# Kernel optimization log

Measured on AMD Instinct MI355X. Metric: run time of the kernel, lower is better.

The kernel has to match this reference:

```python
import jax, jax.numpy as jnp
import numpy as np

SR = 48000.0
HARMONIC_NUM = 8
DIM = HARMONIC_NUM + 1
SINE_AMP = 0.1
NOISE_STD = 0.003
VOICED_THRESHOLD = 0.0


def setup_inputs() -> dict:
    key = jax.random.key(0)
    k1, k2, k3, k4 = jax.random.split(key, 4)
    B, L, upp = 4, 1000, 512
    Lo = L * upp
    f0 = jax.random.uniform(k1, (B, L), dtype=jnp.float32, minval=80.0, maxval=400.0)
    voiced = jax.random.uniform(k2, (B, L)) > 0.2
    f0 = f0 * voiced.astype(jnp.float32)
    rand_ini = jax.random.uniform(k3, (B, DIM), dtype=jnp.float32)
    noise_randn = jax.random.normal(k4, (B, Lo, DIM), dtype=jnp.float32)
    return {"f0": f0, "rand_ini": rand_ini, "noise_randn": noise_randn, "upp": upp}


def _linear_upsample_align_corners(x, upp):
    # x: (B, L, D) -> (B, L*upp, D), matches F.interpolate(mode='linear', align_corners=True)
    B, L, D = x.shape
    Lo = L * upp
    pos = jnp.arange(Lo, dtype=jnp.float32) * (jnp.float32(L - 1) / jnp.float32(Lo - 1))
    i0 = jnp.clip(jnp.floor(pos).astype(jnp.int32), 0, L - 2)
    frac = (pos - i0.astype(jnp.float32))[None, :, None]
    return x[:, i0, :] * (1.0 - frac) + x[:, i0 + 1, :] * frac


def reference(f0, rand_ini, noise_randn, upp):
    B, L = f0.shape
    Lo = L * upp
    # harmonics: f0, 2*f0, ..., DIM*f0  -> (B, L, DIM)
    f0_buf = f0[:, :, None] * jnp.arange(1, DIM + 1, dtype=f0.dtype)
    rad_values = (f0_buf / SR) % 1.0
    # random initial phase, first harmonic fixed at 0
    ri = rand_ini.at[:, 0].set(0.0)
    rad_values = rad_values.at[:, 0, :].add(ri)
    # cumulative phase at frame rate, scaled and upsampled
    tmp_over_one = jnp.cumsum(rad_values, axis=1) * upp
    tmp_over_one = _linear_upsample_align_corners(tmp_over_one, upp)  # (B, Lo, DIM)
    rad_up = jnp.repeat(rad_values, upp, axis=1)  # nearest upsample (B, Lo, DIM)
    tmp_over_one = tmp_over_one % 1.0
    # detect wrap-around and inject -1 phase shift so cumsum stays consistent
    wrap = (tmp_over_one[:, 1:, :] - tmp_over_one[:, :-1, :]) < 0
    cumsum_shift = jnp.concatenate(
        [jnp.zeros((B, 1, DIM), dtype=f0.dtype), -wrap.astype(f0.dtype)], axis=1
    )
    phase = jnp.cumsum(rad_up + cumsum_shift, axis=1)
    sine_waves = jnp.sin(phase * (2.0 * jnp.pi)) * SINE_AMP
    # voiced/unvoiced mask at frame rate, nearest-upsampled
    uv = (f0 > VOICED_THRESHOLD).astype(f0.dtype)[:, :, None]  # (B, L, 1)
    uv = jnp.repeat(uv, upp, axis=1)  # (B, Lo, 1)
    noise_amp = uv * NOISE_STD + (1.0 - uv) * (SINE_AMP / 3.0)
    noise = noise_amp * noise_randn
    sine_waves = sine_waves * uv + noise
    return sine_waves, uv, noise
```

## Files before the change

kernel.cpp:

```cpp
#include <hip/hip_runtime.h>
#include <math.h>

#define DIM 9
#define SINE_AMP 0.1f
#define NOISE_STD 0.003f

typedef float f32x4 __attribute__((ext_vector_type(4)));
typedef float f32x2 __attribute__((ext_vector_type(2)));

__global__ void __launch_bounds__(1024)
phase_scan_kernel(const float* __restrict__ f0,
                  const float* __restrict__ rand_ini,
                  f32x2* __restrict__ rb_out,
                  int B, int L, int upp)
{
    const int bd   = blockIdx.x;
    const int b    = bd / DIM;
    const int d    = bd - b * DIM;
    const int tid  = threadIdx.x;
    const int lane = tid & 63;
    const int wid  = tid >> 6;
    const float hf = (float)(d + 1);
    const float ri = (d == 0) ? 0.0f : rand_ini[b * DIM + d];

    __shared__ double partials[16];
    __shared__ double wave_off[17];

    double carry = 0.0;
    for (int c0 = 0; c0 < L; c0 += 1024) {
        const int l = c0 + tid;
        float r = 0.0f, fv = 0.0f;
        if (l < L) {
            fv = f0[b * L + l];
            r = fmodf(fv * hf / 48000.0f, 1.0f);
            if (l == 0) r += ri;
        }
        const double rd = (double)r;
        double inc = rd;
        #pragma unroll
        for (int off = 1; off < 64; off <<= 1) {
            double t = __shfl_up(inc, off, 64);
            if (lane >= off) inc += t;
        }
        if (lane == 63) partials[wid] = inc;
        __syncthreads();
        if (tid == 0) {
            double run = 0.0;
            #pragma unroll
            for (int w = 0; w < 16; ++w) { wave_off[w] = run; run += partials[w]; }
            wave_off[16] = run;
        }
        __syncthreads();
        if (l < L) {
            const double excl = carry + wave_off[wid] + (inc - rd);
            double bf = excl * (double)upp;
            bf -= floor(bf);
            const bool voiced = fv > 0.0f;
            f32x2 rbv;
            rbv.x = voiced ? r : 0.0f;
            rbv.y = voiced ? (float)bf : 0.0f;
            rb_out[(b * L + l) * DIM + d] = rbv;
        }
        carry += wave_off[16];
        __syncthreads();
    }
}

template <int UPP>
__global__ void __launch_bounds__(256)
sine_gen_kernel(const float* __restrict__ f0,
                const float* __restrict__ noise_randn,
                const f32x2* __restrict__ rb,
                float* __restrict__ out_sine,
                float* __restrict__ out_uv,
                float* __restrict__ out_noise,
                int L, int Lo, int upp)
{
    const unsigned UPPD = (UPP > 0) ? (unsigned)UPP : 1u;
    const unsigned uppv = (UPP > 0) ? (unsigned)UPP : (unsigned)upp;

    const int b   = blockIdx.y;
    const int LoD = Lo * DIM;
    const unsigned n4 = (unsigned)LoD >> 2;
    const long long boff = (long long)b * LoD;

    const f32x4* __restrict__ nz_b    = (const f32x4*)(noise_randn + boff);
    f32x4* __restrict__       sine_b  = (f32x4*)(out_sine + boff);
    f32x4* __restrict__       noise_b = (f32x4*)(out_noise + boff);
    const float*  __restrict__ f0_b   = f0 + b * L;
    const f32x2* __restrict__  rb_b   = rb + b * L * DIM;

    const unsigned tid    = blockIdx.x * blockDim.x + threadIdx.x;
    const unsigned stride = gridDim.x * blockDim.x;

    for (unsigned i4 = tid; i4 < n4; i4 += stride) {
        const unsigned i0 = i4 << 2;
        const f32x4 nr = nz_b[i4];
        unsigned o = i0 / 9u;
        unsigned d = i0 - o * 9u;
        f32x4 sv, nv;
        #pragma unroll
        for (int k = 0; k < 4; ++k) {
            unsigned l, j;
            if (UPP > 0) { l = o / UPPD; j = o - l * UPPD; }
            else         { l = o / (unsigned)upp; j = o - l * (unsigned)upp; }
            const f32x2 rbv = rb_b[l * 9u + d];
            float ph = fmaf((float)(j + 1u), rbv.x, rbv.y);
            ph -= floorf(ph);
            float s;
            asm("v_sin_f32 %0, %1" : "=v"(s) : "v"(ph));
            const float namp = (rbv.x > 0.0f) ? NOISE_STD : (SINE_AMP / 3.0f);
            const float nzv = namp * nr[k];
            nv[k] = nzv;
            sv[k] = fmaf(s, SINE_AMP, nzv);
            if (k < 3) {
                ++d;
                if (d == 9u) { d = 0u; ++o; }
            }
        }
        sine_b[i4]  = sv;
        noise_b[i4] = nv;
    }

    f32x4* __restrict__ uv_b4 = (f32x4*)(out_uv + (long long)b * Lo);
    const unsigned nu4 = (unsigned)Lo >> 2;
    for (unsigned u4 = tid; u4 < nu4; u4 += stride) {
        const unsigned o0 = u4 << 2;
        f32x4 uvv;
        #pragma unroll
        for (int k = 0; k < 4; ++k) {
            const unsigned o = o0 + (unsigned)k;
            const unsigned l = o / uppv;
            uvv[k] = (f0_b[l] > 0.0f) ? 1.0f : 0.0f;
        }
        uv_b4[u4] = uvv;
    }

    if (blockIdx.x == 0 && threadIdx.x < (unsigned)(LoD & 3)) {
        const unsigned rem = (n4 << 2) + threadIdx.x;
        const unsigned o = rem / 9u;
        const unsigned d = rem - o * 9u;
        const unsigned l = o / uppv;
        const unsigned j = o - l * uppv;
        const f32x2 rbv = rb_b[l * 9u + d];
        float ph = fmaf((float)(j + 1u), rbv.x, rbv.y);
        ph -= floorf(ph);
        float s;
        asm("v_sin_f32 %0, %1" : "=v"(s) : "v"(ph));
        const float namp = (rbv.x > 0.0f) ? NOISE_STD : (SINE_AMP / 3.0f);
        const float nzv = namp * ((const float*)nz_b)[rem];
        ((float*)noise_b)[rem] = nzv;
        ((float*)sine_b)[rem]  = fmaf(s, SINE_AMP, nzv);
    }
    if (blockIdx.x == 0 && threadIdx.x < (unsigned)(Lo & 3)) {
        const unsigned o = (nu4 << 2) + threadIdx.x;
        const unsigned l = o / uppv;
        ((float*)uv_b4)[o] = (f0_b[l] > 0.0f) ? 1.0f : 0.0f;
    }
}

extern "C" void kernel_launch(void* const* d_in, const int* in_sizes, int n_in,
                              void* d_out, int out_size, void* d_ws, size_t ws_size,
                              hipStream_t stream)
{
    const float* f0       = (const float*)d_in[0];
    const float* rand_ini = (const float*)d_in[1];
    const float* noise    = (const float*)d_in[2];
    const int B  = in_sizes[1] / DIM;
    const int L  = in_sizes[0] / B;
    const int Lo = in_sizes[2] / (B * DIM);
    const int upp = Lo / L;

    float* out       = (float*)d_out;
    float* out_sine  = out;
    float* out_uv    = out_sine + (long long)B * Lo * DIM;
    float* out_noise = out_uv + (long long)B * Lo;

    f32x2* rb_ws = (f32x2*)d_ws;

    phase_scan_kernel<<<dim3(B * DIM), dim3(1024), 0, stream>>>(
        f0, rand_ini, rb_ws, B, L, upp);

    const int n4 = (Lo * DIM) >> 2;
    int bx = (n4 + 255) / 256;
    if (bx > 1024) bx = 1024;
    dim3 grid(bx, B);
    if (upp == 512) {
        sine_gen_kernel<512><<<grid, dim3(256), 0, stream>>>(
            f0, noise, rb_ws, out_sine, out_uv, out_noise, L, Lo, upp);
    } else {
        sine_gen_kernel<0><<<grid, dim3(256), 0, stream>>>(
            f0, noise, rb_ws, out_sine, out_uv, out_noise, L, Lo, upp);
    }
}
```

Baseline: 44.51 us.

## Fuse phase scan into sine generation with per-block redundant prefix sums

For upp=512, this replaces the two-kernel pipeline (frame-rate phase scan writing to a workspace, then sample generation) with a single fused kernel. Each block recomputes, in double precision, the prefix sum of harmonic phase increments over all frames before its tile. It then builds a small two-row phase table in shared memory and generates the sine, noise and uv outputs for its 1024 elements. This removes one launch and the workspace round trip. In exchange, every block redundantly does O(L·DIM) fmodf and double-precision work, which grows with the tile's position in the sequence.

Measured after the change: 94.58 us. +112.5%, slower.

```diff
diff --git a/kernel.cpp b/kernel.cpp
--- a/kernel.cpp
+++ b/kernel.cpp
@@ -7,6 +7,121 @@
 
 typedef float f32x4 __attribute__((ext_vector_type(4)));
 typedef float f32x2 __attribute__((ext_vector_type(2)));
+
+__global__ void __launch_bounds__(256)
+fused_sine_kernel(const float* __restrict__ f0,
+                  const float* __restrict__ rand_ini,
+                  const float* __restrict__ noise_randn,
+                  float* __restrict__ out_sine,
+                  float* __restrict__ out_uv,
+                  float* __restrict__ out_noise,
+                  int L, int Lo)
+{
+    const int b    = blockIdx.y;
+    const int tid  = threadIdx.x;
+    const int lane = tid & 63, wid = tid >> 6;
+    const int LoD  = Lo * DIM;
+    const unsigned n4 = (unsigned)LoD >> 2;
+
+    const float* __restrict__ f0_b = f0 + b * L;
+
+    const unsigned e0 = (unsigned)blockIdx.x * 1024u;
+    const int l0 = (int)(e0 / (512u * 9u));
+
+    double acc[DIM];
+    #pragma unroll
+    for (int d = 0; d < DIM; ++d) acc[d] = 0.0;
+
+    for (int l = tid; l < l0; l += 256) {
+        const float fv = f0_b[l];
+        #pragma unroll
+        for (int d = 0; d < DIM; ++d) {
+            float r = fmodf(fv * (float)(d + 1) / 48000.0f, 1.0f);
+            if (l == 0) r += (d == 0) ? 0.0f : rand_ini[b * DIM + d];
+            acc[d] += (double)r;
+        }
+    }
+    #pragma unroll
+    for (int d = 0; d < DIM; ++d) {
+        double v = acc[d];
+        #pragma unroll
+        for (int off = 32; off > 0; off >>= 1)
+            v += __shfl_down(v, off, 64);
+        acc[d] = v;
+    }
+    __shared__ double wsum[4][DIM];
+    __shared__ f32x2  tab[2][DIM];
+    if (lane == 0) {
+        #pragma unroll
+        for (int d = 0; d < DIM; ++d) wsum[wid][d] = acc[d];
+    }
+    __syncthreads();
+    if (tid < DIM) {
+        const int d = tid;
+        double S = wsum[0][d] + wsum[1][d] + wsum[2][d] + wsum[3][d];
+        #pragma unroll
+        for (int row = 0; row < 2; ++row) {
+            const int l = l0 + row;
+            f32x2 e; e.x = 0.0f; e.y = 0.0f;
+            if (l < L) {
+                const float fv = f0_b[l];
+                float r = fmodf(fv * (float)(d + 1) / 48000.0f, 1.0f);
+                if (l == 0) r += (d == 0) ? 0.0f : rand_ini[b * DIM + d];
+                double bf = S * 512.0;
+                bf -= floor(bf);
+                if (fv > 0.0f) { e.x = r; e.y = (float)bf; }
+                S += (double)r;
+            }
+            tab[row][d] = e;
+        }
+    }
+    __syncthreads();
+
+    const long long boff = (long long)b * LoD;
+    const f32x4* __restrict__ nz_b    = (const f32x4*)(noise_randn + boff);
+    f32x4* __restrict__       sine_b  = (f32x4*)(out_sine + boff);
+    f32x4* __restrict__       noise_b = (f32x4*)(out_noise + boff);
+
+    const unsigned i4 = (e0 >> 2) + (unsigned)tid;
+    if (i4 < n4) {
+        const f32x4 nr = nz_b[i4];
+        const unsigned rem0 = i4 << 2;
+        unsigned o = rem0 / 9u;
+        unsigned d = rem0 - o * 9u;
+        f32x4 sv, nv;
+        #pragma unroll
+        for (int k = 0; k < 4; ++k) {
+            const unsigned j  = o & 511u;
+            const int     row = (int)(o >> 9) - l0;
+            const f32x2 rbv = tab[row][d];
+            float ph = fmaf((float)(j + 1u), rbv.x, rbv.y);
+            ph -= floorf(ph);
+            float s;
+            asm("v_sin_f32 %0, %1" : "=v"(s) : "v"(ph));
+            const float namp = (rbv.x > 0.0f) ? NOISE_STD : (SINE_AMP / 3.0f);
+            const float nzv  = namp * nr[k];
+            nv[k] = nzv;
+            sv[k] = fmaf(s, SINE_AMP, nzv);
+            if (k < 3) { ++d; if (d == 9u) { d = 0u; ++o; } }
+        }
+        sine_b[i4]  = sv;
+        noise_b[i4] = nv;
+    }
+
+    const unsigned nu4 = (unsigned)Lo >> 2;
+    const unsigned u4  = (unsigned)blockIdx.x * 256u + (unsigned)tid;
+    if (u4 < nu4) {
+        f32x4* __restrict__ uv_b4 = (f32x4*)(out_uv + (long long)b * Lo);
+        const unsigned o0 = u4 << 2;
+        f32x4 uvv;
+        #pragma unroll
+        for (int k = 0; k < 4; ++k) {
+            const unsigned l = (o0 + (unsigned)k) >> 9;
+            uvv[k] = (f0_b[l] > 0.0f) ? 1.0f : 0.0f;
+        }
+        uv_b4[u4] = uvv;
+    }
+}
 
 __global__ void __launch_bounds__(1024)
 phase_scan_kernel(const float* __restrict__ f0,
@@ -66,7 +181,6 @@
     }
 }
 
-template <int UPP>
 __global__ void __launch_bounds__(256)
 sine_gen_kernel(const float* __restrict__ f0,
                 const float* __restrict__ noise_randn,
@@ -76,9 +190,7 @@
                 float* __restrict__ out_noise,
                 int L, int Lo, int upp)
 {
-    const unsigned UPPD = (UPP > 0) ? (unsigned)UPP : 1u;
-    const unsigned uppv = (UPP > 0) ? (unsigned)UPP : (unsigned)upp;
-
+    const unsigned uppv = (unsigned)upp;
     const int b   = blockIdx.y;
     const int LoD = Lo * DIM;
     const unsigned n4 = (unsigned)LoD >> 2;
@@ -101,9 +213,8 @@
         f32x4 sv, nv;
         #pragma unroll
         for (int k = 0; k < 4; ++k) {
-            unsigned l, j;
-            if (UPP > 0) { l = o / UPPD; j = o - l * UPPD; }
-            else         { l = o / (unsigned)upp; j = o - l * (unsigned)upp; }
+            const unsigned l = o / uppv;
+            const unsigned j = o - l * uppv;
             const f32x2 rbv = rb_b[l * 9u + d];
             float ph = fmaf((float)(j + 1u), rbv.x, rbv.y);
             ph -= floorf(ph);
@@ -113,10 +224,7 @@
             const float nzv = namp * nr[k];
             nv[k] = nzv;
             sv[k] = fmaf(s, SINE_AMP, nzv);
-            if (k < 3) {
-                ++d;
-                if (d == 9u) { d = 0u; ++o; }
-            }
+            if (k < 3) { ++d; if (d == 9u) { d = 0u; ++o; } }
         }
         sine_b[i4]  = sv;
         noise_b[i4] = nv;
@@ -129,8 +237,7 @@
         f32x4 uvv;
         #pragma unroll
         for (int k = 0; k < 4; ++k) {
-            const unsigned o = o0 + (unsigned)k;
-            const unsigned l = o / uppv;
+            const unsigned l = (o0 + (unsigned)k) / uppv;
             uvv[k] = (f0_b[l] > 0.0f) ? 1.0f : 0.0f;
         }
         uv_b4[u4] = uvv;
@@ -176,20 +283,20 @@
     float* out_uv    = out_sine + (long long)B * Lo * DIM;
     float* out_noise = out_uv + (long long)B * Lo;
 
-    f32x2* rb_ws = (f32x2*)d_ws;
-
-    phase_scan_kernel<<<dim3(B * DIM), dim3(1024), 0, stream>>>(
-        f0, rand_ini, rb_ws, B, L, upp);
-
-    const int n4 = (Lo * DIM) >> 2;
-    int bx = (n4 + 255) / 256;
-    if (bx > 1024) bx = 1024;
-    dim3 grid(bx, B);
-    if (upp == 512) {
-        sine_gen_kernel<512><<<grid, dim3(256), 0, stream>>>(
+    if (upp == 512 && (Lo & 3) == 0) {
+        const int LoD = Lo * DIM;
+        const int bx  = (LoD + 1023) / 1024;
+        fused_sine_kernel<<<dim3(bx, B), dim3(256), 0, stream>>>(
+            f0, rand_ini, noise, out_sine, out_uv, out_noise, L, Lo);
+    } else {
+        f32x2* rb_ws = (f32x2*)d_ws;
+        phase_scan_kernel<<<dim3(B * DIM), dim3(1024), 0, stream>>>(
+            f0, rand_ini, rb_ws, B, L, upp);
+        const int n4 = (Lo * DIM) >> 2;
+        int bx = (n4 + 255) / 256;
+        if (bx > 1024) bx = 1024;
+        dim3 grid(bx, B);
+        sine_gen_kernel<<<grid, dim3(256), 0, stream>>>(
             f0, noise, rb_ws, out_sine, out_uv, out_noise, L, Lo, upp);
-    } else {
-        sine_gen_kernel<0><<<grid, dim3(256), 0, stream>>>(
-            f0, noise, rb_ws, out_sine, out_uv, out_noise, L, Lo, upp);
     }
 }
```

## Add upp=512 sine kernel with shared-memory frame table and non-persistent grid

Applied to the files above, without the earlier changes.

Adds a specialised kernel for upp=512 in which each block covers 2048 elements, which span at most two frames. The block stages the phase/rate pairs for those two frames in shared memory, so the per-element loads come from LDS instead of global or cache. The old grid-stride loop capped at 1024 blocks becomes one block per 2048-element chunk, with two float4 vectors per thread and no loop. The uv output is folded into the same launch, and the generic path loses its template specialisation.

Result: slower. 46.57 us (+4.6%).

```diff
diff --git a/kernel.cpp b/kernel.cpp
--- a/kernel.cpp
+++ b/kernel.cpp
@@ -66,7 +66,86 @@
     }
 }
 
-template <int UPP>
+__global__ void __launch_bounds__(256)
+sine_gen512_kernel(const float* __restrict__ f0,
+                   const float* __restrict__ noise_randn,
+                   const f32x2* __restrict__ rb,
+                   float* __restrict__ out_sine,
+                   float* __restrict__ out_uv,
+                   float* __restrict__ out_noise,
+                   int L, int Lo)
+{
+    const int b   = blockIdx.y;
+    const int tid = threadIdx.x;
+    const int LoD = Lo * DIM;
+    const unsigned n4  = (unsigned)LoD >> 2;
+    const unsigned nu4 = (unsigned)Lo >> 2;
+
+    const long long boff = (long long)b * LoD;
+    const f32x4* __restrict__ nz_b    = (const f32x4*)(noise_randn + boff);
+    f32x4* __restrict__       sine_b  = (f32x4*)(out_sine + boff);
+    f32x4* __restrict__       noise_b = (f32x4*)(out_noise + boff);
+    const float* __restrict__ f0_b    = f0 + b * L;
+    const f32x2* __restrict__ rb_b    = rb + b * L * DIM;
+
+    const unsigned e0 = (unsigned)blockIdx.x * 2048u;
+    const int l0 = (int)(e0 / 4608u);
+    __shared__ f32x2 tab[2][DIM];
+    if (tid < 2 * DIM) {
+        const int row = tid / DIM, d = tid - row * DIM;
+        const int l = l0 + row;
+        f32x2 e; e.x = 0.0f; e.y = 0.0f;
+        if (l < L) e = rb_b[l * DIM + d];
+        tab[row][d] = e;
+    }
+    __syncthreads();
+
+    const unsigned p   = (unsigned)blockIdx.x * 256u + (unsigned)tid;
+    const unsigned i4a = p << 1, i4b = i4a + 1u;
+    if (i4a < n4) {
+        const bool hasb = (i4b < n4);
+        const f32x4 nra = nz_b[i4a];
+        f32x4 nrb;
+        if (hasb) nrb = nz_b[i4b];
+
+        const unsigned rem0 = i4a << 2;
+        unsigned o = rem0 / 9u;
+        unsigned d = rem0 - o * 9u;
+        f32x4 sv0, nv0, sv1, nv1;
+        #pragma unroll
+        for (int k = 0; k < 8; ++k) {
+            const unsigned j  = o & 511u;
+            const int    row  = (int)(o >> 9) - l0;
+            const f32x2 rbv = tab[row][d];
+            float ph = fmaf((float)(j + 1u), rbv.x, rbv.y);
+            ph -= floorf(ph);
+            float s;
+            asm("v_sin_f32 %0, %1" : "=v"(s) : "v"(ph));
+            const float namp = (rbv.x > 0.0f) ? NOISE_STD : (SINE_AMP / 3.0f);
+            const float nz   = namp * ((k < 4) ? nra[k & 3] : nrb[k & 3]);
+            const float sn   = fmaf(s, SINE_AMP, nz);
+            if (k < 4) { nv0[k & 3] = nz; sv0[k & 3] = sn; }
+            else       { nv1[k & 3] = nz; sv1[k & 3] = sn; }
+            if (k < 7) { ++d; if (d == 9u) { d = 0u; ++o; } }
+        }
+        sine_b[i4a]  = sv0;
+        noise_b[i4a] = nv0;
+        if (hasb) { sine_b[i4b] = sv1; noise_b[i4b] = nv1; }
+    }
+
+    if (p < nu4) {
+        f32x4* __restrict__ uv_b4 = (f32x4*)(out_uv + (long long)b * Lo);
+        const unsigned o0 = p << 2;
+        f32x4 uvv;
+        #pragma unroll
+        for (int k = 0; k < 4; ++k) {
+            const unsigned l = (o0 + (unsigned)k) >> 9;
+            uvv[k] = (f0_b[l] > 0.0f) ? 1.0f : 0.0f;
+        }
+        uv_b4[p] = uvv;
+    }
+}
+
 __global__ void __launch_bounds__(256)
 sine_gen_kernel(const float* __restrict__ f0,
                 const float* __restrict__ noise_randn,
@@ -76,9 +155,7 @@
                 float* __restrict__ out_noise,
                 int L, int Lo, int upp)
 {
-    const unsigned UPPD = (UPP > 0) ? (unsigned)UPP : 1u;
-    const unsigned uppv = (UPP > 0) ? (unsigned)UPP : (unsigned)upp;
-
+    const unsigned uppv = (unsigned)upp;
     const int b   = blockIdx.y;
     const int LoD = Lo * DIM;
     const unsigned n4 = (unsigned)LoD >> 2;
@@ -101,9 +178,8 @@
         f32x4 sv, nv;
         #pragma unroll
         for (int k = 0; k < 4; ++k) {
-            unsigned l, j;
-            if (UPP > 0) { l = o / UPPD; j = o - l * UPPD; }
-            else         { l = o / (unsigned)upp; j = o - l * (unsigned)upp; }
+            const unsigned l = o / uppv;
+            const unsigned j = o - l * uppv;
             const f32x2 rbv = rb_b[l * 9u + d];
             float ph = fmaf((float)(j + 1u), rbv.x, rbv.y);
             ph -= floorf(ph);
@@ -113,10 +189,7 @@
             const float nzv = namp * nr[k];
             nv[k] = nzv;
             sv[k] = fmaf(s, SINE_AMP, nzv);
-            if (k < 3) {
-                ++d;
-                if (d == 9u) { d = 0u; ++o; }
-            }
+            if (k < 3) { ++d; if (d == 9u) { d = 0u; ++o; } }
         }
         sine_b[i4]  = sv;
         noise_b[i4] = nv;
@@ -129,8 +202,7 @@
         f32x4 uvv;
         #pragma unroll
         for (int k = 0; k < 4; ++k) {
-            const unsigned o = o0 + (unsigned)k;
-            const unsigned l = o / uppv;
+            const unsigned l = (o0 + (unsigned)k) / uppv;
             uvv[k] = (f0_b[l] > 0.0f) ? 1.0f : 0.0f;
         }
         uv_b4[u4] = uvv;
@@ -181,15 +253,17 @@
     phase_scan_kernel<<<dim3(B * DIM), dim3(1024), 0, stream>>>(
         f0, rand_ini, rb_ws, B, L, upp);
 
-    const int n4 = (Lo * DIM) >> 2;
-    int bx = (n4 + 255) / 256;
-    if (bx > 1024) bx = 1024;
-    dim3 grid(bx, B);
     if (upp == 512) {
-        sine_gen_kernel<512><<<grid, dim3(256), 0, stream>>>(
+        const int LoD = Lo * DIM;
+        const int bx  = (LoD + 2047) / 2048;
+        sine_gen512_kernel<<<dim3(bx, B), dim3(256), 0, stream>>>(
+            f0, noise, rb_ws, out_sine, out_uv, out_noise, L, Lo);
+    } else {
+        const int n4 = (Lo * DIM) >> 2;
+        int bx = (n4 + 255) / 256;
+        if (bx > 1024) bx = 1024;
+        dim3 grid(bx, B);
+        sine_gen_kernel<<<grid, dim3(256), 0, stream>>>(
             f0, noise, rb_ws, out_sine, out_uv, out_noise, L, Lo, upp);
-    } else {
-        sine_gen_kernel<0><<<grid, dim3(256), 0, stream>>>(
-            f0, noise, rb_ws, out_sine, out_uv, out_noise, L, Lo, upp);
-    }
-}
+    }
+}
```
